# Kernel optimization log

Measured on AMD Instinct MI355X. Metric: run time of the kernel, lower is better.

Reference implementation:

```python
import jax, jax.numpy as jnp
import numpy as np
from jax import lax

B, S, D = 8, 96, 768
R, RSEQ, TAG = 24, 8, 3


def setup_inputs() -> dict:
    key = jax.random.key(0)
    k0, k1, k2, k3 = jax.random.split(key, 4)
    encoded_text = jax.random.normal(k0, (B, S, D), jnp.float32)
    rel_types_encoded = jax.random.normal(k1, (R, RSEQ, D), jnp.float32)
    proj_W = jax.random.normal(k2, (2 * D, 3 * D), jnp.float32) * 0.02
    proj_b = jnp.zeros((3 * D,), jnp.float32)
    rel_W = jax.random.normal(k3, (3 * D, R * TAG), jnp.float32) * 0.02
    rel_b = jnp.zeros((R * TAG,), jnp.float32)
    return {
        "encoded_text": encoded_text,
        "rel_types_encoded": rel_types_encoded,
        "proj_W": proj_W,
        "proj_b": proj_b,
        "rel_W": rel_W,
        "rel_b": rel_b,
    }


def _refine(enc, rel_types):
    """Faithful vectorized version of the nested python loops in
    get_encoded_text: for each sample i, R sequential cross-attention
    updates on matrix_b using matrix_a = rel_types_encoded[i] (the
    original code indexes with i, reusing the same matrix_a each step).
    enc: [Bsz, S, D]; rel_types: [R, RSEQ, D].
    """
    Bsz = enc.shape[0]
    d = enc.shape[-1]
    scale = 1.0 / jnp.sqrt(jnp.asarray(d, enc.dtype))
    num_steps = rel_types.shape[0]  # loop runs rel_types_encoded.size(0) times
    A_batch = rel_types[:Bsz]  # matrix_a = rel_types_encoded[i]

    def per_sample(b0, A):  # b0: [S, D], A: [RSEQ, D]
        def step(b, _):
            scores = (A @ b.T) * scale            # [RSEQ, S]
            w = jax.nn.softmax(scores, axis=-1)    # softmax over seq
            return b + w.T @ A, None               # matrix_b += matrix_c
        bf, _ = lax.scan(step, b0, None, length=num_steps)
        return bf

    return jax.vmap(per_sample)(enc, A_batch)


def reference(encoded_text, rel_types_encoded, proj_W, proj_b, rel_W, rel_b):
    enc = _refine(encoded_text, rel_types_encoded)  # [B, S, D]
    Bsz, seq, d = enc.shape
    rel_num = rel_types_encoded.shape[0]
    tag_size = rel_W.shape[1] // rel_num

    # projection(cat(head, tail)) == head @ Wh + tail @ Wt + b; avoid
    # materializing the [B, S*S, 2D] concat (same math as the original).
    Wh, Wt = proj_W[:d], proj_W[d:]
    Hh = enc @ Wh                                   # [B, S, 3D] head part
    Ht = enc @ Wt                                   # [B, S, 3D] tail part
    pairs = Hh[:, :, None, :] + Ht[:, None, :, :] + proj_b  # [B, S, S, 3D]
    pairs = jax.nn.relu(pairs)
    triple = pairs.reshape(Bsz, seq * seq, 3 * d) @ rel_W + rel_b
    triple = triple.reshape(Bsz, seq, seq, rel_num, tag_size)
    return jnp.transpose(triple, (0, 4, 3, 1, 2))  # [B, tag, rel, S, S]
```

## Files before the change

kernel.cpp:

```cpp
#include <hip/hip_runtime.h>
#include <hip/hip_bf16.h>
#include <math.h>
#include <stdint.h>
#include <string.h>

#define BB 8
#define SS 96
#define DD 768
#define RR 24
#define RSEQ 8
#define TAG 3
#define D3 2304
#define NC 72

typedef __attribute__((ext_vector_type(8))) short bf16x8;
typedef __attribute__((ext_vector_type(4))) float f32x4;
typedef _Float16 f16x8 __attribute__((ext_vector_type(8)));
typedef _Float16 f16x2 __attribute__((ext_vector_type(2)));

typedef __attribute__((address_space(3))) uint8_t lds_u8;
typedef const __attribute__((address_space(1))) uint8_t glb_u8;
static __device__ __forceinline__ void glld16(const void* g, void* l) {
  __builtin_amdgcn_global_load_lds((glb_u8*)g, (lds_u8*)l, 16, 0, 0);
}

static __device__ inline uint32_t pkrhu(float lo, float hi) {
  uint32_t a, b;
  memcpy(&a, &lo, 4);
  memcpy(&b, &hi, 4);
  return __builtin_amdgcn_perm(b + 0x8000u, a + 0x8000u, 0x07060302u);
}
static __device__ inline uint32_t pkrne(float lo, float hi) {
  uint32_t a, b;
  memcpy(&a, &lo, 4);
  memcpy(&b, &hi, 4);
  a += 0x7FFFu + ((a >> 16) & 1u);
  b += 0x7FFFu + ((b >> 16) & 1u);
  return (a >> 16) | (b & 0xFFFF0000u);
}
static __device__ inline uint32_t pkf16(float lo, float hi) {
  union { f16x2 h; uint32_t u; } r;
  r.h[0] = (_Float16)lo;
  r.h[1] = (_Float16)hi;
  return r.u;
}
static __device__ inline uint16_t f16b(float v) {
  union { _Float16 h; uint16_t u; } r;
  r.h = (_Float16)v;
  return r.u;
}

__global__ __launch_bounds__(256) void k_prep0(const float* __restrict__ relW,
                                               uint16_t* __restrict__ Wb,
                                               const float* __restrict__ projW,
                                               uint16_t* __restrict__ Tp,
                                               const float* __restrict__ enc,
                                               const float* __restrict__ rel,
                                               float* __restrict__ SG) {
  __shared__ __align__(16) char smem[24704];
  const int blk = blockIdx.x;
  const int t = threadIdx.x;

  if (blk < 36) {
    float* tile = (float*)smem;
    const int k0 = blk * 64;
    const float* src = relW + (size_t)k0 * NC;
    for (int e = t; e < 64 * NC / 4; e += 256) ((float4*)tile)[e] = ((const float4*)src)[e];
    __syncthreads();
    for (int u = t; u < 80 * 16; u += 256) {
      const int n = u >> 4, kq = (u & 15) * 4;
      uint2 w = {0u, 0u};
      if (n < NC) {
        w.x = pkf16(tile[(kq + 0) * NC + n], tile[(kq + 1) * NC + n]);
        w.y = pkf16(tile[(kq + 2) * NC + n], tile[(kq + 3) * NC + n]);
      }
      *(uint2*)&Wb[(size_t)n * D3 + k0 + kq] = w;
    }
  } else if (blk < 900) {
    const int bx = blk - 36;
    float (*tile)[65] = (float(*)[65])smem;
    const int c0 = (bx % 36) * 64;
    const int r0 = (bx / 36) * 64;
    {
      const int tr = t >> 4;
      const int tc4 = (t & 15) * 4;
#pragma unroll
      for (int p = 0; p < 4; ++p) {
        const int r = tr + p * 16;
        const float4 v = *(const float4*)&projW[(size_t)(r0 + r) * D3 + c0 + tc4];
        tile[r][tc4 + 0] = v.x;
        tile[r][tc4 + 1] = v.y;
        tile[r][tc4 + 2] = v.z;
        tile[r][tc4 + 3] = v.w;
      }
    }
    __syncthreads();
    {
      const int cc = t >> 4;
      const int rr4 = (t & 15) * 4;
#pragma unroll
      for (int p = 0; p < 4; ++p) {
        const int c = cc + p * 16;
        uint2 w;
        w.x = pkrne(tile[rr4 + 0][c], tile[rr4 + 1][c]);
        w.y = pkrne(tile[rr4 + 2][c], tile[rr4 + 3][c]);
        *(uint2*)&Tp[(size_t)(c0 + c) * (2 * DD) + r0 + rr4] = w;
      }
    }
  } else {
    const int idx = blk - 900;
    const int b = idx >> 4;
    const int d0 = (idx & 15) * 48;
    float (*AsF)[48] = (float(*)[48])smem;

    if (t < 96) {
      const int r = t / 12, q4 = (t % 12) * 4;
      *(float4*)&AsF[r][q4] = *(const float4*)&rel[((size_t)b * RSEQ + r) * DD + d0 + q4];
    }
    __syncthreads();

    for (int e = t; e < RSEQ * (SS + RSEQ); e += 256) {
      const int r = e & 7, s = e >> 3;
      const float* row = (s < SS) ? (enc + ((size_t)b * SS + s) * DD + d0) : &AsF[s - SS][0];
      float a0 = 0.f, a1 = 0.f, a2 = 0.f, a3 = 0.f;
#pragma unroll
      for (int d = 0; d < 48; d += 4) {
        const float4 rv = *(const float4*)&row[d];
        a0 += AsF[r][d + 0] * rv.x;
        a1 += AsF[r][d + 1] * rv.y;
        a2 += AsF[r][d + 2] * rv.z;
        a3 += AsF[r][d + 3] * rv.w;
      }
      atomicAdd(&SG[((size_t)b * RSEQ + r) * 104 + s], (a0 + a1) + (a2 + a3));
    }
  }
}

__global__ __launch_bounds__(256) void k_refS(const float* __restrict__ SG,
                                              float* __restrict__ Pst) {
  const int b = blockIdx.x;
  const int t = threadIdx.x;
  __shared__ float S0[RSEQ][SS];
  __shared__ float G[RSEQ][RSEQ];
  __shared__ float P[RSEQ][SS];
  __shared__ float sc[RSEQ][SS];
  const float scale = 0.036084391824351613f;

  for (int e = t; e < RSEQ * 104; e += 256) {
    const int r = e / 104, c = e % 104;
    const float v = SG[(size_t)b * RSEQ * 104 + e];
    if (c < SS) S0[r][c] = v;
    else G[r][c - SS] = v;
  }
  for (int e = t; e < RSEQ * SS; e += 256) ((float*)P)[e] = 0.f;
  __syncthreads();

  const int wave = t >> 6, lane = t & 63;
  for (int step = 0; step < RR; ++step) {
    for (int e = t; e < RSEQ * SS; e += 256) {
      const int r = e / SS, s = e % SS;
      float acc = S0[r][s];
#pragma unroll
      for (int r2 = 0; r2 < RSEQ; ++r2) acc += G[r][r2] * P[r2][s];
      sc[r][s] = acc * scale;
    }
    __syncthreads();
#pragma unroll
    for (int rr = 0; rr < 2; ++rr) {
      const int r = wave * 2 + rr;
      const float m1 = sc[r][lane];
      const float m2 = (lane < 32) ? sc[r][lane + 64] : -1e30f;
      float mx = fmaxf(m1, m2);
#pragma unroll
      for (int o = 32; o > 0; o >>= 1) mx = fmaxf(mx, __shfl_xor(mx, o, 64));
      const float e1 = __expf(m1 - mx);
      const float e2 = (lane < 32) ? __expf(m2 - mx) : 0.f;
      float sm = e1 + e2;
#pragma unroll
      for (int o = 32; o > 0; o >>= 1) sm += __shfl_xor(sm, o, 64);
      const float inv = 1.f / sm;
      P[r][lane] += e1 * inv;
      if (lane < 32) P[r][lane + 64] += e2 * inv;
    }
    __syncthreads();
  }

  for (int e = t; e < RSEQ * SS; e += 256) Pst[(size_t)b * RSEQ * SS + e] = ((float*)P)[e];
}

__global__ __launch_bounds__(256) void k_refB(const float* __restrict__ enc,
                                              const float* __restrict__ rel,
                                              const float* __restrict__ Pst,
                                              uint16_t* __restrict__ encRb) {
  const int blk = blockIdx.x;
  const int b = blk / 12;
  const int s0 = (blk % 12) * 8;
  const int t = threadIdx.x;
  __shared__ float As[RSEQ][DD + 4];
  __shared__ float Pl[RSEQ][8];

  const float* Ag = rel + (size_t)b * RSEQ * DD;
  for (int e = t; e < RSEQ * DD / 4; e += 256) {
    const int r = (e * 4) / DD, d = (e * 4) % DD;
    *(float4*)&As[r][d] = *(const float4*)&Ag[e * 4];
  }
  if (t < RSEQ * 8) {
    const int r = t >> 3, sl = t & 7;
    Pl[r][sl] = Pst[(size_t)b * RSEQ * SS + r * SS + s0 + sl];
  }
  __syncthreads();

  const float* Eb = enc + ((size_t)b * SS + s0) * DD;
  uint16_t* Ob = encRb + ((size_t)b * SS + s0) * DD;
  for (int e = t; e < 8 * DD / 4; e += 256) {
    const int sl = (e * 4) / DD, d = (e * 4) % DD;
    float4 v = ((const float4*)Eb)[e];
#pragma unroll
    for (int r = 0; r < RSEQ; ++r) {
      const float p = Pl[r][sl];
      v.x += p * As[r][d + 0];
      v.y += p * As[r][d + 1];
      v.z += p * As[r][d + 2];
      v.w += p * As[r][d + 3];
    }
    uint2 w;
    w.x = pkrhu(v.x, v.y);
    w.y = pkrhu(v.z, v.w);
    *(uint2*)&Ob[e * 4] = w;
  }
}

__global__ __launch_bounds__(256, 4) void k_proj(const uint16_t* __restrict__ Ab,
                                                 const uint16_t* __restrict__ Bt,
                                                 const float* __restrict__ pb,
                                                 uint16_t* __restrict__ Hh16,
                                                 uint16_t* __restrict__ Htf) {
  const int m0 = blockIdx.x * 64;
  const int gn0 = blockIdx.y * 64;
  const bool isH = gn0 < D3;
  const int n0 = isH ? gn0 : gn0 - D3;
  const int halfk = isH ? 0 : DD;
  const int t = threadIdx.x, w = t >> 6, lane = t & 63;
  const int wm = w >> 1, wn = w & 1;
  const int lm = lane & 15, q = lane >> 4;

  __shared__ __align__(16) uint16_t As[64 * 72];
  __shared__ __align__(16) uint16_t Bs[64 * 72];

  const char* rp[5];
  char* lp[5];
#pragma unroll
  for (int r = 0; r < 5; ++r) {
    const int idx = w + 4 * r;
    rp[r] = nullptr;
    lp[r] = nullptr;
    if (idx < 18) {
      const int ii = (idx < 9) ? idx : idx - 9;
      const int beta = ii * 1024 + lane * 16;
      const int elem = beta >> 1;
      const int row = elem / 72;
      int o = elem - row * 72;
      if (o >= 64) o = 0;
      if (idx < 9) {
        rp[r] = (const char*)(Ab + (size_t)(m0 + row) * DD + o);
        lp[r] = (char*)As + ii * 1024;
      } else {
        rp[r] = (const char*)(Bt + (size_t)(n0 + row) * (2 * DD) + halfk + o);
        lp[r] = (char*)Bs + ii * 1024;
      }
    }
  }

  f32x4 acc[2][2];
#pragma unroll
  for (int a = 0; a < 2; ++a)
#pragma unroll
    for (int c = 0; c < 2; ++c) acc[a][c] = (f32x4){0.f, 0.f, 0.f, 0.f};

  for (int k0 = 0; k0 < DD; k0 += 64) {
    __syncthreads();
#pragma unroll
    for (int r = 0; r < 5; ++r)
      if (rp[r]) glld16(rp[r] + 2 * k0, lp[r]);
    __syncthreads();
#pragma unroll
    for (int kk = 0; kk < 2; ++kk) {
      const int ko = kk * 32 + q * 8;
      bf16x8 af[2], bf[2];
#pragma unroll
      for (int mt = 0; mt < 2; ++mt)
        af[mt] = *(const bf16x8*)&As[(wm * 32 + mt * 16 + lm) * 72 + ko];
#pragma unroll
      for (int nt = 0; nt < 2; ++nt)
        bf[nt] = *(const bf16x8*)&Bs[(wn * 32 + nt * 16 + lm) * 72 + ko];
#pragma unroll
      for (int nt = 0; nt < 2; ++nt)
#pragma unroll
        for (int mt = 0; mt < 2; ++mt)
          acc[mt][nt] = __builtin_amdgcn_mfma_f32_16x16x32_bf16(af[mt], bf[nt], acc[mt][nt], 0, 0, 0);
    }
  }

#pragma unroll
  for (int nt = 0; nt < 2; ++nt) {
    const int ncol = n0 + wn * 32 + nt * 16 + lm;
    const int mrow = m0 + wm * 32 + q * 4;
    uint16_t* dst = isH ? Hh16 : Htf;
    const float bias = isH ? pb[ncol] : 0.f;
#pragma unroll
    for (int mt = 0; mt < 2; ++mt)
#pragma unroll
      for (int r = 0; r < 4; ++r)
        dst[(size_t)(mrow + mt * 16 + r) * D3 + ncol] = f16b(acc[mt][nt][r] + bias);
  }
}

#define HTS_B (96 * 144)
#define WOFF (HTS_B / 2)

__global__ __launch_bounds__(256, 3) void k_pairs(const uint16_t* __restrict__ Hh,
                                                  const uint16_t* __restrict__ Htb,
                                                  const uint16_t* __restrict__ Wb,
                                                  const float* __restrict__ relb,
                                                  float* __restrict__ out) {
  const int bi = blockIdx.x;
  const int b = bi / SS, i = bi % SS;
  const int t = threadIdx.x;
  const int w = t >> 6, lane = t & 63;
  const int lm = lane & 15, q = lane >> 4;
  const int wm = w >> 1, wn = w & 1;
  const int ntn = wn ? 2 : 3;

  __shared__ __align__(16) uint16_t Hrow[2560];
  __shared__ __align__(16) uint16_t Stg[12800];

  {
    const char* hh = (const char*)(Hh + (size_t)bi * D3);
#pragma unroll
    for (int r = 0; r < 2; ++r) {
      const int idx = w + 4 * r;
      if (idx < 5) glld16(hh + idx * 1024 + lane * 16, (char*)Hrow + idx * 1024);
    }
  }

  const char* rp[7];
#pragma unroll
  for (int r = 0; r < 7; ++r) {
    const int idx = w + 4 * r;
    rp[r] = nullptr;
    if (idx < 25) {
      const int beta = idx * 1024 + lane * 16;
      int elem, row, o;
      const char* base;
      if (beta < HTS_B) {
        elem = beta >> 1;
        row = elem / 72;
        o = elem - row * 72;
        base = (const char*)(Htb + ((size_t)b * SS + row) * D3);
      } else {
        elem = (beta - HTS_B) >> 1;
        row = elem / 72;
        o = elem - row * 72;
        base = (const char*)(Wb + (size_t)row * D3);
      }
      if (o >= 64) o = 0;
      rp[r] = base + 2 * o;
    }
  }

  f32x4 acc[3][3];
#pragma unroll
  for (int mt = 0; mt < 3; ++mt)
#pragma unroll
    for (int nt = 0; nt < 3; ++nt) acc[mt][nt] = (f32x4){0.f, 0.f, 0.f, 0.f};

  const f16x8 zro = {0, 0, 0, 0, 0, 0, 0, 0};

  for (int k0 = 0; k0 < D3; k0 += 64) {
    __syncthreads();
#pragma unroll
    for (int r = 0; r < 7; ++r) {
      const int idx = w + 4 * r;
      if (idx < 25) glld16(rp[r] + 2 * k0, (char*)Stg + idx * 1024);
    }
    __syncthreads();

#pragma unroll
    for (int kk = 0; kk < 2; ++kk) {
      const int ko = kk * 32 + q * 8;
      const f16x8 hv = *(const f16x8*)&Hrow[k0 + ko];
      f16x8 af[3];
#pragma unroll
      for (int mt = 0; mt < 3; ++mt) {
        const int j = wm * 48 + mt * 16 + lm;
        const f16x8 s = *(const f16x8*)&Stg[j * 72 + ko] + hv;
        af[mt] = __builtin_elementwise_max(s, zro);
      }
#pragma unroll
      for (int nt = 0; nt < 3; ++nt) {
        if (nt < ntn) {
          const int n = (wn * 3 + nt) * 16 + lm;
          const f16x8 bfv = *(const f16x8*)&Stg[WOFF + n * 72 + ko];
#pragma unroll
          for (int mt = 0; mt < 3; ++mt)
            acc[mt][nt] = __builtin_amdgcn_mfma_f32_16x16x32_f16(af[mt], bfv, acc[mt][nt], 0, 0, 0);
        }
      }
    }
  }

#pragma unroll
  for (int nt = 0; nt < 3; ++nt) {
    if (nt < ntn) {
      const int c = (wn * 3 + nt) * 16 + lm;
      if (c < NC) {
        const float rb = relb[c];
        const int rr = c / 3, tg = c % 3;
#pragma unroll
        for (int mt = 0; mt < 3; ++mt) {
          const int j0 = wm * 48 + mt * 16 + q * 4;
          float* base = out + ((((size_t)b * TAG + tg) * RR + rr) * SS + i) * SS + j0;
          float4 o;
          o.x = acc[mt][nt][0] + rb;
          o.y = acc[mt][nt][1] + rb;
          o.z = acc[mt][nt][2] + rb;
          o.w = acc[mt][nt][3] + rb;
          *(float4*)base = o;
        }
      }
    }
  }
}

extern "C" void kernel_launch(void* const* d_in, const int* in_sizes, int n_in,
                              void* d_out, int out_size, void* d_ws, size_t ws_size,
                              hipStream_t stream) {
  const float* enc   = (const float*)d_in[0];
  const float* rel   = (const float*)d_in[1];
  const float* projW = (const float*)d_in[2];
  const float* projb = (const float*)d_in[3];
  const float* relW  = (const float*)d_in[4];
  const float* relb  = (const float*)d_in[5];
  float* out = (float*)d_out;

  uint16_t* Hh16 = (uint16_t*)d_ws;
  uint16_t* Htf  = Hh16 + (size_t)DD * D3 + 256;
  uint16_t* Wb   = Htf + (size_t)DD * D3;
  uint16_t* Tp   = Wb + (size_t)96 * D3;
  uint16_t* Ab   = Tp + (size_t)D3 * 2 * DD;
  float* Pst = (float*)(Ab + (size_t)DD * DD);
  float* SG = Pst + (size_t)BB * RSEQ * SS;

  hipMemsetAsync(SG, 0, (size_t)BB * RSEQ * 104 * sizeof(float), stream);
  k_prep0<<<1028, 256, 0, stream>>>(relW, Wb, projW, Tp, enc, rel, SG);
  k_refS<<<BB, 256, 0, stream>>>(SG, Pst);
  k_refB<<<96, 256, 0, stream>>>(enc, rel, Pst, Ab);
  k_proj<<<dim3(12, 72), 256, 0, stream>>>(Ab, Tp, projb, Hh16, Htf);
  k_pairs<<<BB * SS, 256, 0, stream>>>(Hh16, Htf, Wb, relb, out);
}
```

Measured before the change: 190.8 us.

## Process three head rows per block in k_pairs with double-buffered staging

Restructures the pair kernel so each 192-thread block handles three head rows (one per wave), sharing each staged Ht/W tile across all three. That cuts repeated global loads of Ht and rel_W per head row by three. The K loop is double-buffered, so the next chunk's global-to-LDS load overlaps the current MFMA work and only one barrier remains per iteration. The cost is a larger register tile (6x5 accumulators per wave), more LDS, only 256 blocks, and launch bounds of 1, which lowers occupancy.

```diff
diff --git a/kernel.cpp b/kernel.cpp
--- a/kernel.cpp
+++ b/kernel.cpp
@@ -317,36 +317,36 @@
 
 #define HTS_B (96 * 144)
 #define WOFF (HTS_B / 2)
-
-__global__ __launch_bounds__(256, 3) void k_pairs(const uint16_t* __restrict__ Hh,
+#define NKC 36
+
+__global__ __launch_bounds__(192, 1) void k_pairs(const uint16_t* __restrict__ Hh,
                                                   const uint16_t* __restrict__ Htb,
                                                   const uint16_t* __restrict__ Wb,
                                                   const float* __restrict__ relb,
                                                   float* __restrict__ out) {
-  const int bi = blockIdx.x;
-  const int b = bi / SS, i = bi % SS;
+  const int blk = blockIdx.x;
+  const int b = blk >> 5, ii = blk & 31;
   const int t = threadIdx.x;
   const int w = t >> 6, lane = t & 63;
   const int lm = lane & 15, q = lane >> 4;
-  const int wm = w >> 1, wn = w & 1;
-  const int ntn = wn ? 2 : 3;
-
-  __shared__ __align__(16) uint16_t Hrow[2560];
-  __shared__ __align__(16) uint16_t Stg[12800];
+  const int i = ii * 3 + w;
+
+  __shared__ __align__(16) uint16_t Hr[7168];
+  __shared__ __align__(16) uint16_t Stg[2][12800];
 
   {
-    const char* hh = (const char*)(Hh + (size_t)bi * D3);
-#pragma unroll
-    for (int r = 0; r < 2; ++r) {
-      const int idx = w + 4 * r;
-      if (idx < 5) glld16(hh + idx * 1024 + lane * 16, (char*)Hrow + idx * 1024);
-    }
-  }
-
-  const char* rp[7];
-#pragma unroll
-  for (int r = 0; r < 7; ++r) {
-    const int idx = w + 4 * r;
+    const char* hh = (const char*)(Hh + ((size_t)b * SS + ii * 3) * D3);
+#pragma unroll
+    for (int r = 0; r < 5; ++r) {
+      const int idx = w + 3 * r;
+      if (idx < 14) glld16(hh + idx * 1024 + lane * 16, (char*)Hr + idx * 1024);
+    }
+  }
+
+  const char* rp[9];
+#pragma unroll
+  for (int r = 0; r < 9; ++r) {
+    const int idx = w + 3 * r;
     rp[r] = nullptr;
     if (idx < 25) {
       const int beta = idx * 1024 + lane * 16;
@@ -368,65 +368,68 @@
     }
   }
 
-  f32x4 acc[3][3];
-#pragma unroll
-  for (int mt = 0; mt < 3; ++mt)
-#pragma unroll
-    for (int nt = 0; nt < 3; ++nt) acc[mt][nt] = (f32x4){0.f, 0.f, 0.f, 0.f};
+#pragma unroll
+  for (int r = 0; r < 9; ++r)
+    if (rp[r]) glld16(rp[r], (char*)Stg[0] + (w + 3 * r) * 1024);
+  __syncthreads();
+
+  f32x4 acc[6][5];
+#pragma unroll
+  for (int mt = 0; mt < 6; ++mt)
+#pragma unroll
+    for (int nt = 0; nt < 5; ++nt) acc[mt][nt] = (f32x4){0.f, 0.f, 0.f, 0.f};
 
   const f16x8 zro = {0, 0, 0, 0, 0, 0, 0, 0};
 
-  for (int k0 = 0; k0 < D3; k0 += 64) {
-    __syncthreads();
-#pragma unroll
-    for (int r = 0; r < 7; ++r) {
-      const int idx = w + 4 * r;
-      if (idx < 25) glld16(rp[r] + 2 * k0, (char*)Stg + idx * 1024);
-    }
-    __syncthreads();
-
+  for (int tc = 0; tc < NKC; ++tc) {
+    const uint16_t* S = &Stg[tc & 1][0];
+    if (tc + 1 < NKC) {
+      char* dst = (char*)Stg[(tc + 1) & 1];
+      const size_t koff = (size_t)128 * (tc + 1);
+#pragma unroll
+      for (int r = 0; r < 9; ++r)
+        if (rp[r]) glld16(rp[r] + koff, dst + (w + 3 * r) * 1024);
+    }
+    const int k0 = tc * 64;
 #pragma unroll
     for (int kk = 0; kk < 2; ++kk) {
       const int ko = kk * 32 + q * 8;
-      const f16x8 hv = *(const f16x8*)&Hrow[k0 + ko];
-      f16x8 af[3];
-#pragma unroll
-      for (int mt = 0; mt < 3; ++mt) {
-        const int j = wm * 48 + mt * 16 + lm;
-        const f16x8 s = *(const f16x8*)&Stg[j * 72 + ko] + hv;
+      const f16x8 hv = *(const f16x8*)&Hr[w * D3 + k0 + ko];
+      f16x8 af[6];
+#pragma unroll
+      for (int mt = 0; mt < 6; ++mt) {
+        const f16x8 s = *(const f16x8*)&S[(mt * 16 + lm) * 72 + ko] + hv;
         af[mt] = __builtin_elementwise_max(s, zro);
       }
-#pragma unroll
-      for (int nt = 0; nt < 3; ++nt) {
-        if (nt < ntn) {
-          const int n = (wn * 3 + nt) * 16 + lm;
-          const f16x8 bfv = *(const f16x8*)&Stg[WOFF + n * 72 + ko];
-#pragma unroll
-          for (int mt = 0; mt < 3; ++mt)
-            acc[mt][nt] = __builtin_amdgcn_mfma_f32_16x16x32_f16(af[mt], bfv, acc[mt][nt], 0, 0, 0);
-        }
-      }
-    }
-  }
-
-#pragma unroll
-  for (int nt = 0; nt < 3; ++nt) {
-    if (nt < ntn) {
-      const int c = (wn * 3 + nt) * 16 + lm;
-      if (c < NC) {
-        const float rb = relb[c];
-        const int rr = c / 3, tg = c % 3;
-#pragma unroll
-        for (int mt = 0; mt < 3; ++mt) {
-          const int j0 = wm * 48 + mt * 16 + q * 4;
-          float* base = out + ((((size_t)b * TAG + tg) * RR + rr) * SS + i) * SS + j0;
-          float4 o;
-          o.x = acc[mt][nt][0] + rb;
-          o.y = acc[mt][nt][1] + rb;
-          o.z = acc[mt][nt][2] + rb;
-          o.w = acc[mt][nt][3] + rb;
-          *(float4*)base = o;
-        }
+      f16x8 bfv[5];
+#pragma unroll
+      for (int nt = 0; nt < 5; ++nt)
+        bfv[nt] = *(const f16x8*)&S[WOFF + (nt * 16 + lm) * 72 + ko];
+#pragma unroll
+      for (int nt = 0; nt < 5; ++nt)
+#pragma unroll
+        for (int mt = 0; mt < 6; ++mt)
+          acc[mt][nt] = __builtin_amdgcn_mfma_f32_16x16x32_f16(af[mt], bfv[nt], acc[mt][nt], 0, 0, 0);
+    }
+    __syncthreads();
+  }
+
+#pragma unroll
+  for (int nt = 0; nt < 5; ++nt) {
+    const int c = nt * 16 + lm;
+    if (c < NC) {
+      const float rb = relb[c];
+      const int rr = c / 3, tg = c % 3;
+#pragma unroll
+      for (int mt = 0; mt < 6; ++mt) {
+        const int j0 = mt * 16 + q * 4;
+        float* base = out + ((((size_t)b * TAG + tg) * RR + rr) * SS + i) * SS + j0;
+        float4 o;
+        o.x = acc[mt][nt][0] + rb;
+        o.y = acc[mt][nt][1] + rb;
+        o.z = acc[mt][nt][2] + rb;
+        o.w = acc[mt][nt][3] + rb;
+        *(float4*)base = o;
       }
     }
   }
@@ -456,5 +459,5 @@
   k_refS<<<BB, 256, 0, stream>>>(SG, Pst);
   k_refB<<<96, 256, 0, stream>>>(enc, rel, Pst, Ab);
   k_proj<<<dim3(12, 72), 256, 0, stream>>>(Ab, Tp, projb, Hh16, Htf);
-  k_pairs<<<BB * SS, 256, 0, stream>>>(Hh16, Htf, Wb, relb, out);
-}
+  k_pairs<<<256, 192, 0, stream>>>(Hh16, Htf, Wb, relb, out);
+}
```

Result: slower. 202.8 us (+6.3%).
